# Kernel optimization log

Hardware: AMD Instinct MI355X
Metric: run time of the kernel (lower is better)

The kernel has to match this reference:

```python
import jax, jax.numpy as jnp
import numpy as np

B, S, HID = 2, 2048, 2048
H, D_NOPE, D_ROPE = 16, 128, 64
KV_LORA = 192            # forced so v_head dim == pad_hd == 128 (see torch view)
NUM_SLOTS, MAX_LEN = 8, 2048
SCALE = D_NOPE ** -0.5


def setup_inputs() -> dict:
    key = jax.random.key(0)
    ks = jax.random.split(key, 4)
    return {
        "hidden_states": jax.random.normal(ks[0], (B, S, HID), jnp.float32),
        "Wq": jax.random.normal(ks[1], (H * (D_NOPE + D_ROPE), HID), jnp.float32) * 0.02,
        "Wkv": jax.random.normal(ks[2], (KV_LORA + D_ROPE, HID), jnp.float32) * 0.02,
        "Wo": jax.random.normal(ks[3], (HID, H * D_NOPE), jnp.float32) * 0.02,
        "k_cache": jnp.zeros((NUM_SLOTS, MAX_LEN, 1, D_NOPE), jnp.float32),
        "v_cache": jnp.zeros((NUM_SLOTS, MAX_LEN, 1, D_NOPE), jnp.float32),
        "slot_mapping": jnp.arange(B, dtype=jnp.int32),
        "kv_start_indices": jnp.zeros((B,), jnp.int32),
        "seq_lens": jnp.full((B,), S, jnp.int32),
        "positions": jnp.arange(S, dtype=jnp.int32),
    }


def reference(hidden_states, Wq, Wkv, Wo, k_cache, v_cache,
              slot_mapping, kv_start_indices, seq_lens, positions):
    # q / low-rank kv projections (nn.Linear convention: x @ W.T)
    q = (hidden_states @ Wq.T).reshape(B, S, H, D_NOPE + D_ROPE)
    q_nope = q[..., :D_NOPE]                       # [B,S,H,128]
    kv = hidden_states @ Wkv.T                     # [B,S,256]
    k = kv[..., :D_NOPE][:, :, None, :]            # [B,S,1,128] single latent kv head
    v = kv[..., D_NOPE:][:, :, None, :]            # [B,S,1,128]

    # paged KV-cache scatter (prefill: kv_start_indices == 0, write [0:S))
    k_cache = k_cache.at[slot_mapping, :S].set(k)
    v_cache = v_cache.at[slot_mapping, :S].set(v)

    # gather history back (max_l = seq_lens.max() == S at prefill, static)
    k_hist = k_cache[slot_mapping, :S]             # [B,L,1,128]
    v_hist = v_cache[slot_mapping, :S]

    # MQA attention: sum over singleton kv-head axis == repeat_interleave broadcast
    scores = jnp.einsum('bshd,blod->bhsl', q_nope, k_hist) * SCALE  # [B,H,S,L]
    causal = jnp.triu(jnp.ones((S, S), bool), k=1)  # diagonal = start(0)+1
    scores = jnp.where(causal[None, None], -jnp.inf, scores)
    attn = jax.nn.softmax(scores, axis=-1)
    out = jnp.einsum('bhsl,blod->bshd', attn, v_hist)  # [B,S,H,128]
    out = out.reshape(B, S, H * D_NOPE)
    return out @ Wo.T
```

## Files before the change

### kernel.cpp

```cpp
#include <hip/hip_runtime.h>
#include <hip/hip_bf16.h>
#include <stdint.h>


typedef __attribute__((ext_vector_type(4))) float f32x4;
typedef __attribute__((ext_vector_type(8))) short bf16x8;
typedef __attribute__((ext_vector_type(4))) short bf16x4;

__device__ __forceinline__ unsigned short f2bf(float f) {
    union { float f; unsigned u; } v; v.f = f;
    unsigned u = v.u;
    return (unsigned short)((u + 0x7fffu + ((u >> 16) & 1u)) >> 16);
}

__device__ __forceinline__ short bf_rn(float f) {
    __hip_bfloat16 h = __float2bfloat16(f);
    short s; __builtin_memcpy(&s, &h, 2); return s;
}

__device__ __forceinline__ float exp2_raw(float x) {
#if __has_builtin(__builtin_amdgcn_exp2f)
    return __builtin_amdgcn_exp2f(x);
#else
    return exp2f(x);
#endif
}

#define MFMA32(a,b,c) __builtin_amdgcn_mfma_f32_16x16x32_bf16((a),(b),(c),0,0,0)
#if defined(__HIP_DEVICE_COMPILE__)
#define MFMA16(a,b,c) __builtin_amdgcn_mfma_f32_16x16x16bf16_1k((a),(b),(c),0,0,0)
#else
#define MFMA16(a,b,c) (c)
#endif

#define GLD_LDS16(g,l) __builtin_amdgcn_global_load_lds( \
    (const __attribute__((address_space(1))) unsigned int*)(g), \
    (__attribute__((address_space(3))) unsigned int*)(l), 16, 0, 0)

__global__ void cvt_all(const float* __restrict__ in, unsigned short* __restrict__ out, int n4) {
    const int stride = gridDim.x * blockDim.x;
    for (int i = blockIdx.x * blockDim.x + threadIdx.x; i < n4; i += stride) {
        float4 v = ((const float4*)in)[i];
        ushort4 r;
        r.x = f2bf(v.x); r.y = f2bf(v.y); r.z = f2bf(v.z); r.w = f2bf(v.w);
        ((ushort4*)out)[i] = r;
    }
}

__global__ void cvt_wqkv(const float* __restrict__ wq, const float* __restrict__ wkv,
                         unsigned short* __restrict__ out) {
    const int row = blockIdx.x;
    const bool isq = (row < 2048);
    const float sc = isq ? 0.1275174331181861f : 1.0f;
    const float* srcp = isq ? (wq + (long)((row >> 7) * 192 + (row & 127)) * 2048)
                            : (wkv + (long)(row - 2048) * 2048);
    const float4* ip = (const float4*)srcp;
    ushort4* op = (ushort4*)(out + (long)row * 2048);
    for (int i = threadIdx.x; i < 512; i += 256) {
        float4 v = ip[i];
        ushort4 r;
        r.x = f2bf(v.x * sc); r.y = f2bf(v.y * sc);
        r.z = f2bf(v.z * sc); r.w = f2bf(v.w * sc);
        op[i] = r;
    }
}

__global__ void transpose_v(const unsigned short* __restrict__ qkv, unsigned short* __restrict__ vt) {
    __shared__ unsigned short tile[32][33];
    const int b = blockIdx.z, dt = blockIdx.y, st = blockIdx.x;
    const int x = threadIdx.x, y = threadIdx.y;
    const int s0 = st * 32, d0 = dt * 32;
    #pragma unroll
    for (int i = 0; i < 4; ++i)
        tile[y + i * 8][x] = qkv[((long)(b * 2048 + s0 + y + i * 8)) * 2304 + 2176 + d0 + x];
    __syncthreads();
    #pragma unroll
    for (int i = 0; i < 4; ++i)
        vt[((long)(b * 128 + d0 + y + i * 8)) * 2048 + s0 + x] = tile[x][y + i * 8];
}

template<int OUT_BF16>
__global__ __launch_bounds__(256, 2)
void gemm_bt(const unsigned short* __restrict__ A,
             const unsigned short* __restrict__ B,
             void* __restrict__ Cp, int M, int N, int K) {
    __shared__ unsigned short As[128 * 64];
    __shared__ unsigned short Bs[128 * 64];
    const int t = threadIdx.x;
    const int wave = t >> 6, lane = t & 63;
    const int wr = wave >> 1, wc = wave & 1;
    const int l15 = lane & 15, l4 = lane >> 4;
    const long m0 = blockIdx.y * 128L, n0 = blockIdx.x * 128L;
    f32x4 acc[4][4] = {};
    for (int k0 = 0; k0 < K; k0 += 64) {
        #pragma unroll
        for (int it = 0; it < 4; ++it) {
            const int c = it * 4 + wave;
            const int e = c * 64 + lane;
            const int row = e >> 3;
            const int col = (e & 7) << 3;
            GLD_LDS16(A + (m0 + row) * K + k0 + col, As + c * 512);
            GLD_LDS16(B + (n0 + row) * K + k0 + col, Bs + c * 512);
        }
        __syncthreads();
        #pragma unroll
        for (int ks = 0; ks < 2; ++ks) {
            bf16x8 af[4], bfr[4];
            #pragma unroll
            for (int m = 0; m < 4; ++m)
                af[m] = *(const bf16x8*)(As + (wr * 64 + m * 16 + l15) * 64 + ks * 32 + l4 * 8);
            #pragma unroll
            for (int n = 0; n < 4; ++n)
                bfr[n] = *(const bf16x8*)(Bs + (wc * 64 + n * 16 + l15) * 64 + ks * 32 + l4 * 8);
            #pragma unroll
            for (int m = 0; m < 4; ++m)
                #pragma unroll
                for (int n = 0; n < 4; ++n)
                    acc[m][n] = MFMA32(af[m], bfr[n], acc[m][n]);
        }
        __syncthreads();
    }
    #pragma unroll
    for (int m = 0; m < 4; ++m)
        #pragma unroll
        for (int n = 0; n < 4; ++n) {
            const long rg = m0 + wr * 64 + m * 16 + l4 * 4;
            const long cg = n0 + wc * 64 + n * 16 + l15;
            #pragma unroll
            for (int i = 0; i < 4; ++i) {
                float v = acc[m][n][i];
                if (OUT_BF16) ((unsigned short*)Cp)[(rg + i) * N + cg] = f2bf(v);
                else          ((float*)Cp)[(rg + i) * N + cg] = v;
            }
        }
}

__global__ __launch_bounds__(256, 2)
void attn_fused(const unsigned short* __restrict__ QKV,
                const unsigned short* __restrict__ VT,
                unsigned short* __restrict__ AO) {
    __shared__ unsigned short Ks[2][64 * 128];
    __shared__ unsigned short Vs[2][128 * 64];
    const int t = threadIdx.x;
    const int wave = t >> 6, lane = t & 63;
    const int l15 = lane & 15, l4 = lane >> 4;
    const int bid = blockIdx.x;
    const int p = bid >> 4;
    const int hgb = bid & 15;
    const int hg = hgb >> 1, b = hgb & 1;
    const int h = hg * 2 + (wave >> 1);
    const int qsub = wave & 1;
    const long rowB = (long)b * 2048;

    const unsigned short* ksrc[4];
    const unsigned short* vsrc[4];
    #pragma unroll
    for (int it = 0; it < 4; ++it) {
        const int c = it * 4 + wave;
        const int krow = c * 4 + (lane >> 4);
        const int ksp = (lane & 15) ^ (krow & 15);
        ksrc[it] = QKV + (rowB + krow) * 2304 + 2048 + ksp * 8;
        const int vd = c * 8 + (lane >> 3);
        const int vsp = (lane & 7) ^ (vd & 7);
        vsrc[it] = VT + ((long)b * 128 + vd) * 2048 + vsp * 8;
    }

#define STAGE(bufi, jj0) do { \
    _Pragma("unroll") \
    for (int it = 0; it < 4; ++it) { \
        const int c = it * 4 + wave; \
        GLD_LDS16(ksrc[it] + (long)(jj0) * 2304, &Ks[bufi][c * 512]); \
        GLD_LDS16(vsrc[it] + (jj0), &Vs[bufi][c * 512]); \
    } \
} while (0)

    for (int ph = 0; ph < 2; ++ph) {
        const int qt = ph ? p : (63 - p);
        const int q0 = qt * 32;
        const int q0w = q0 + qsub * 16;
        const int nt = (qt >> 1) + 1;

        bf16x8 qf[4];
        {
            const unsigned short* qp = QKV + (rowB + q0w + l15) * 2304 + h * 128;
            #pragma unroll
            for (int kb = 0; kb < 4; ++kb)
                qf[kb] = *(const bf16x8*)(qp + kb * 32 + l4 * 8);
        }

        f32x4 o[8] = {};
        float lsum = 0.f;

        STAGE(0, 0);
        int cur = 0;

        for (int tt = 0; tt < nt; ++tt) {
            const int j0 = tt * 64;
            asm volatile("s_waitcnt vmcnt(0)" ::: "memory");
            __builtin_amdgcn_s_barrier();
            if (tt + 1 < nt) STAGE(cur ^ 1, j0 + 64);

            const unsigned short* ksBase = cur ? &Ks[1][0] : &Ks[0][0];
            f32x4 st[4];
            __builtin_amdgcn_s_setprio(1);
            #pragma unroll
            for (int jkv = 0; jkv < 4; ++jkv) {
                const unsigned short* krp = ksBase + (jkv * 16 + l15) * 128;
                f32x4 s0 = {};
                #pragma unroll
                for (int kb = 0; kb < 4; ++kb) {
                    const int slot = (kb * 4 + l4) ^ l15;
                    bf16x8 kf = *(const bf16x8*)(krp + slot * 8);
                    s0 = MFMA32(kf, qf[kb], s0);
                }
                st[jkv] = s0;
            }
            __builtin_amdgcn_s_setprio(0);

            if (tt + 1 == nt) {
                const int qrow = q0w + l15;
                #pragma unroll
                for (int jkv = 0; jkv < 4; ++jkv)
                    #pragma unroll
                    for (int i = 0; i < 4; ++i) {
                        const int kpos = j0 + jkv * 16 + l4 * 4 + i;
                        if (kpos > qrow) st[jkv][i] = -3.0e38f;
                    }
            }
            float ps = 0.f;
            bf16x4 pa[4];
            #pragma unroll
            for (int jkv = 0; jkv < 4; ++jkv) {
                float p0 = exp2_raw(st[jkv][0]);
                float p1 = exp2_raw(st[jkv][1]);
                float p2 = exp2_raw(st[jkv][2]);
                float p3 = exp2_raw(st[jkv][3]);
                ps += (p0 + p1) + (p2 + p3);
#if defined(__HIP_DEVICE_COMPILE__)
                unsigned r0, r1;
                asm("v_cvt_pk_bf16_f32 %0, %1, %2" : "=v"(r0) : "v"(p0), "v"(p1));
                asm("v_cvt_pk_bf16_f32 %0, %1, %2" : "=v"(r1) : "v"(p2), "v"(p3));
                union { unsigned u[2]; bf16x4 v; } cvt;
                cvt.u[0] = r0; cvt.u[1] = r1;
                pa[jkv] = cvt.v;
#else
                bf16x4 v = { bf_rn(p0), bf_rn(p1), bf_rn(p2), bf_rn(p3) };
                pa[jkv] = v;
#endif
            }
            lsum += ps;

            const unsigned short* vsBase = cur ? &Vs[1][0] : &Vs[0][0];
            __builtin_amdgcn_s_setprio(1);
            #pragma unroll
            for (int dj = 0; dj < 8; ++dj) {
                const int d = dj * 16 + l15;
                const unsigned short* vrow = vsBase + d * 64;
                const int dsw = (d & 7) << 3;
                #pragma unroll
                for (int jkv = 0; jkv < 4; ++jkv) {
                    bf16x4 vf = *(const bf16x4*)(vrow + ((jkv * 16 + l4 * 4) ^ dsw));
                    o[dj] = MFMA16(pa[jkv], vf, o[dj]);
                }
            }
            __builtin_amdgcn_s_setprio(0);
            cur ^= 1;
        }

        float lrow = lsum;
        lrow += __shfl_xor(lrow, 16);
        lrow += __shfl_xor(lrow, 32);
        float il[4];
        #pragma unroll
        for (int i = 0; i < 4; ++i)
            il[i] = 1.0f / __shfl(lrow, l4 * 4 + i);
        #pragma unroll
        for (int dj = 0; dj < 8; ++dj)
            #pragma unroll
            for (int i = 0; i < 4; ++i) {
                const long qrow = rowB + q0w + l4 * 4 + i;
                AO[qrow * 2048 + h * 128 + dj * 16 + l15] = (unsigned short)bf_rn(o[dj][i] * il[i]);
            }
        __syncthreads();
    }
#undef STAGE
}

extern "C" void kernel_launch(void* const* d_in, const int* in_sizes, int n_in,
                              void* d_out, int out_size, void* d_ws, size_t ws_size,
                              hipStream_t stream) {
    const float* hs  = (const float*)d_in[0];
    const float* Wq  = (const float*)d_in[1];
    const float* Wkv = (const float*)d_in[2];
    const float* Wo  = (const float*)d_in[3];
    char* ws = (char*)d_ws;
    unsigned short* h_bf   = (unsigned short*)(ws + 0);
    unsigned short* wqkv_bf= (unsigned short*)(ws + 16777216);
    unsigned short* wo_bf  = (unsigned short*)(ws + 26214400);
    unsigned short* qkv_bf = (unsigned short*)(ws + 34603008);
    unsigned short* vt_bf  = (unsigned short*)(ws + 53477376);
    unsigned short* ao_bf  = (unsigned short*)(ws + 54525952);
    float* out = (float*)d_out;

    cvt_all <<<2048, 256, 0, stream>>>(hs, h_bf, 2097152);
    cvt_all <<<2048, 256, 0, stream>>>(Wo, wo_bf, 1048576);
    cvt_wqkv<<<2304, 256, 0, stream>>>(Wq, Wkv, wqkv_bf);

    gemm_bt<1><<<dim3(18, 32), 256, 0, stream>>>(h_bf, wqkv_bf, qkv_bf, 4096, 2304, 2048);
    transpose_v<<<dim3(64, 4, 2), dim3(32, 8), 0, stream>>>(qkv_bf, vt_bf);
    attn_fused<<<dim3(512, 1, 1), 256, 0, stream>>>(qkv_bf, vt_bf, ao_bf);
    gemm_bt<0><<<dim3(16, 32), 256, 0, stream>>>(ao_bf, wo_bf, out, 4096, 2048, 2048);
}
```

Measured before the change: 191.3 us.

## Double-buffer GEMM LDS tiles with XOR swizzle and block-index swizzle

```diff
diff --git a/kernel.cpp b/kernel.cpp
--- a/kernel.cpp
+++ b/kernel.cpp
@@ -84,42 +84,82 @@
 void gemm_bt(const unsigned short* __restrict__ A,
              const unsigned short* __restrict__ B,
              void* __restrict__ Cp, int M, int N, int K) {
-    __shared__ unsigned short As[128 * 64];
-    __shared__ unsigned short Bs[128 * 64];
+    __shared__ unsigned short As[2][128 * 64];
+    __shared__ unsigned short Bs[2][128 * 64];
     const int t = threadIdx.x;
     const int wave = t >> 6, lane = t & 63;
     const int wr = wave >> 1, wc = wave & 1;
     const int l15 = lane & 15, l4 = lane >> 4;
-    const long m0 = blockIdx.y * 128L, n0 = blockIdx.x * 128L;
+
+    const int nbx = gridDim.x;
+    const int nwg = nbx * gridDim.y;
+    const int borig = blockIdx.y * nbx + blockIdx.x;
+    const int bswz = (borig & 7) * (nwg >> 3) + (borig >> 3);
+    const long m0 = (bswz / nbx) * 128L, n0 = (bswz % nbx) * 128L;
+
+    const unsigned short* asrc[4];
+    const unsigned short* bsrc[4];
+    #pragma unroll
+    for (int it = 0; it < 4; ++it) {
+        const int c = it * 4 + wave;
+        const int row = c * 8 + (lane >> 3);
+        const int gsw = (lane & 7) ^ (row & 7);
+        asrc[it] = A + (m0 + row) * K + gsw * 8;
+        bsrc[it] = B + (n0 + row) * K + gsw * 8;
+    }
+
+#define GSTAGE(bufi, kt) do { \
+    _Pragma("unroll") \
+    for (int it = 0; it < 4; ++it) { \
+        const int c = it * 4 + wave; \
+        GLD_LDS16(asrc[it] + (kt) * 64, &As[bufi][c * 512]); \
+        GLD_LDS16(bsrc[it] + (kt) * 64, &Bs[bufi][c * 512]); \
+    } \
+} while (0)
+
     f32x4 acc[4][4] = {};
-    for (int k0 = 0; k0 < K; k0 += 64) {
-        #pragma unroll
-        for (int it = 0; it < 4; ++it) {
-            const int c = it * 4 + wave;
-            const int e = c * 64 + lane;
-            const int row = e >> 3;
-            const int col = (e & 7) << 3;
-            GLD_LDS16(A + (m0 + row) * K + k0 + col, As + c * 512);
-            GLD_LDS16(B + (n0 + row) * K + k0 + col, Bs + c * 512);
-        }
-        __syncthreads();
+    const int nk = K >> 6;
+    GSTAGE(0, 0);
+    int cur = 0;
+    for (int kt = 0; kt < nk; ++kt) {
+        __builtin_amdgcn_s_barrier();
+        if (kt + 1 < nk) {
+            GSTAGE(cur ^ 1, kt + 1);
+            asm volatile("s_waitcnt vmcnt(8)" ::: "memory");
+        } else {
+            asm volatile("s_waitcnt vmcnt(0)" ::: "memory");
+        }
+        __builtin_amdgcn_s_barrier();
+
+        const unsigned short* as = &As[cur][0];
+        const unsigned short* bs = &Bs[cur][0];
+        __builtin_amdgcn_s_setprio(1);
         #pragma unroll
         for (int ks = 0; ks < 2; ++ks) {
             bf16x8 af[4], bfr[4];
             #pragma unroll
-            for (int m = 0; m < 4; ++m)
-                af[m] = *(const bf16x8*)(As + (wr * 64 + m * 16 + l15) * 64 + ks * 32 + l4 * 8);
-            #pragma unroll
-            for (int n = 0; n < 4; ++n)
-                bfr[n] = *(const bf16x8*)(Bs + (wc * 64 + n * 16 + l15) * 64 + ks * 32 + l4 * 8);
+            for (int m = 0; m < 4; ++m) {
+                const int row = wr * 64 + m * 16 + l15;
+                const int slot = (ks * 4 + l4) ^ (row & 7);
+                af[m] = *(const bf16x8*)(as + row * 64 + slot * 8);
+            }
+            #pragma unroll
+            for (int n = 0; n < 4; ++n) {
+                const int row = wc * 64 + n * 16 + l15;
+                const int slot = (ks * 4 + l4) ^ (row & 7);
+                bfr[n] = *(const bf16x8*)(bs + row * 64 + slot * 8);
+            }
             #pragma unroll
             for (int m = 0; m < 4; ++m)
                 #pragma unroll
                 for (int n = 0; n < 4; ++n)
                     acc[m][n] = MFMA32(af[m], bfr[n], acc[m][n]);
         }
-        __syncthreads();
-    }
+        __builtin_amdgcn_s_setprio(0);
+        cur ^= 1;
+    }
+#undef GSTAGE
+
     #pragma unroll
     for (int m = 0; m < 4; ++m)
         #pragma unroll
```

After: 188.5 us. About the same (-1.5%).
